# Optimization experiments

Measured on AMD Instinct MI355X. Metric: run time of the kernel, lower is better.

## Reference

```python
import jax, jax.numpy as jnp
import numpy as np

H = 128          # hidden_channels
MID = 64         # middle_channels
NH = 8           # num_heads
HD = H // NH     # head_dim
NS = 20000       # source nodes
NT = 20000       # target nodes
E = 320000       # edges
CUT = 5.0        # cosine cutoff radius
SPHE = 3 * 2 ** 2   # num_radial * num_spherical**2 = 12
TORS = 3 * 2        # num_radial * num_spherical = 6

silu = jax.nn.silu


def setup_inputs() -> dict:
    key = jax.random.key(0)
    ks = jax.random.split(key, 40)
    w = lambda k, shp, s=0.05: (jax.random.normal(k, shp, dtype=jnp.float32) * s)
    inp = {
        "x_s": jax.random.normal(ks[0], (NS, H), dtype=jnp.float32),
        "x_t": jax.random.normal(ks[1], (NT, H), dtype=jnp.float32),
        "edge_index": jnp.stack([
            jax.random.randint(ks[2], (E,), 0, NS),
            jax.random.randint(ks[3], (E,), 0, NT)]).astype(jnp.int32),
        "edge_attr": jax.random.normal(ks[4], (E, H), dtype=jnp.float32),
        "sphe_emb": jax.random.normal(ks[5], (E, SPHE), dtype=jnp.float32),
        "torsion_emb": jax.random.normal(ks[6], (E, TORS), dtype=jnp.float32),
        "dist": jax.random.uniform(ks[7], (E,), dtype=jnp.float32) * 6.0,
        # sphe_proj / torsion_proj (bias-free two-layer MLPs)
        "Ws1": w(ks[8], (SPHE, MID)), "Ws2": w(ks[9], (MID, H)),
        "Wt1": w(ks[10], (TORS, MID)), "Wt2": w(ks[11], (MID, H)),
        # attention projections
        "Wq": w(ks[12], (H, H)), "bq": jnp.zeros((H,), jnp.float32),
        "Wk": w(ks[13], (H, H)), "bk": jnp.zeros((H,), jnp.float32),
        "Wv": w(ks[14], (H, H)), "bv": jnp.zeros((H,), jnp.float32),
        "Wdk": w(ks[15], (H, H)), "bdk": jnp.zeros((H,), jnp.float32),
        "Wdv": w(ks[16], (H, H)), "bdv": jnp.zeros((H,), jnp.float32),
        "Wo_att": w(ks[17], (H, H)), "bo_att": jnp.zeros((H,), jnp.float32),
        # message projections
        "Ws_msg": w(ks[18], (H, 2 * H)), "bs_msg": jnp.zeros((2 * H,), jnp.float32),
        "Wcat_msg": w(ks[19], (2 * H, H)),
        "Wo_msg": w(ks[20], (H, 2 * H)), "bo_msg": jnp.zeros((2 * H,), jnp.float32),
        # final proj (conv_type='inter' -> input is concat([h_t, msg]) of width 2H)
        "Wfinal": w(ks[21], (2 * H, H)), "bfinal": jnp.zeros((H,), jnp.float32),
        # edge update (BaseConv, with_update_edge=True)
        "Wf": w(ks[22], (H, 3 * H)), "bf": jnp.zeros((3 * H,), jnp.float32),
        "Wcat_f": w(ks[23], (2 * H, H)), "bcat_f": jnp.zeros((H,), jnp.float32),
    }
    return inp


def reference(x_s, x_t, edge_index, edge_attr, sphe_emb, torsion_emb, dist,
              Ws1, Ws2, Wt1, Wt2, Wq, bq, Wk, bk, Wv, bv, Wdk, bdk, Wdv, bdv,
              Wo_att, bo_att, Ws_msg, bs_msg, Wcat_msg, Wo_msg, bo_msg,
              Wfinal, bfinal, Wf, bf, Wcat_f, bcat_f):
    src, tgt = edge_index[0], edge_index[1]

    # geometric edge embeddings: [E, H]
    d1 = (sphe_emb @ Ws1) @ Ws2
    d2 = (torsion_emb @ Wt1) @ Wt2

    # multi-head q/k/v
    q = (x_t @ Wq + bq).reshape(-1, NH, HD)
    k = (x_s @ Wk + bk).reshape(-1, NH, HD)
    v = (x_s @ Wv + bv).reshape(-1, NH, HD)
    dk = silu(edge_attr @ Wdk + bdk).reshape(-1, NH, HD)
    dv = silu(edge_attr @ Wdv + bdv).reshape(-1, NH, HD)

    # message: gather per-edge, attention-weighted values
    attn = (q[tgt] * k[src] * dk).sum(-1)                 # [E, NH]
    cut = 0.5 * (jnp.cos(jnp.pi * dist / CUT) + 1.0) * (dist < CUT)
    attn = silu(attn) * cut[:, None]
    v_j = (v[src] * dv * attn[:, :, None]).reshape(-1, H)  # [E, H]
    v_j = silu(v_j @ Wo_att + bo_att)
    s = silu(v_j @ Ws_msg + bs_msg)
    s1, s2 = s[:, :H], s[:, H:]
    d_ji = jnp.concatenate([s1 * d1, s2 * d2], axis=1)      # [E, 2H]

    # scatter-add aggregation to target nodes
    s_msg = jax.ops.segment_sum(v_j, tgt, num_segments=NT)   # [NT, H]
    d_msg = jax.ops.segment_sum(d_ji, tgt, num_segments=NT) @ Wcat_msg  # [NT, H]

    # edge update (BaseConv.edge_update)
    f = silu(edge_attr @ Wf + bf)
    f1, f2, f3 = f[:, :H], f[:, H:2 * H], f[:, 2 * H:]
    f_ji = f1 + silu(jnp.concatenate([f2 * d1, f3 * d2], axis=1) @ Wcat_f + bcat_f)

    # node update (conv_type='inter')
    o = s_msg @ Wo_msg + bo_msg
    s_msg1, s_msg2 = o[:, :H], o[:, H:]
    h_t = silu(jnp.concatenate([x_t, s_msg1 + s_msg2 * d_msg], axis=1) @ Wfinal + bfinal)
    return (h_t, f_ji)
```

## Files before the change

### kernel.cpp

```cpp
#include <hip/hip_runtime.h>
#include <math.h>

static constexpr int H    = 128;
static constexpr int MID  = 64;
static constexpr int NS   = 20000;
static constexpr int NT   = 20000;
static constexpr int EDG  = 320000;
static constexpr int SPH  = 12;
static constexpr int TOR  = 6;
static constexpr int TS   = 132;

typedef unsigned long long u64;
typedef unsigned int u32;
typedef unsigned short ushort_t;

using bf8   = __attribute__((ext_vector_type(8))) short;
using f32x4 = __attribute__((ext_vector_type(4))) float;

__device__ __forceinline__ float sil(float x) {
  return x / (1.0f + __expf(-x));
}

__device__ __forceinline__ ushort_t f2bf(float x) {
  u32 u = __float_as_uint(x);
  u32 r = u + 0x7FFFu + ((u >> 16) & 1u);
  return (ushort_t)(r >> 16);
}
__device__ __forceinline__ float bf2f(ushort_t h) {
  return __uint_as_float(((u32)h) << 16);
}

__device__ __forceinline__ bf8 ld_lds_frag(const char* base, u32 b0, u32 b1) {
  union { u64 u[2]; bf8 v; } X;
  X.u[0] = *(const u64*)(base + b0);
  X.u[1] = *(const u64*)(base + b1);
  return X.v;
}
__device__ __forceinline__ bf8 ld_g_frag(const ushort_t* p) {
  union { u64 u[2]; bf8 v; } X;
  X.u[0] = *(const u64*)(p);
  X.u[1] = *(const u64*)(p + 16);
  return X.v;
}

template<int K>
__device__ __forceinline__ void kloop32(const float* __restrict__ W, int ldw,
                                        const float* xr, float* acc) {
  #pragma unroll 2
  for (int i0 = 0; i0 < K; i0 += 4) {
    float4 a4 = *(const float4*)(xr + i0);
    const float* w = W + i0 * ldw;
    #pragma unroll
    for (int j = 0; j < 32; ++j) acc[j] = fmaf(a4.x, w[j], acc[j]);
    w += ldw;
    #pragma unroll
    for (int j = 0; j < 32; ++j) acc[j] = fmaf(a4.y, w[j], acc[j]);
    w += ldw;
    #pragma unroll
    for (int j = 0; j < 32; ++j) acc[j] = fmaf(a4.z, w[j], acc[j]);
    w += ldw;
    #pragma unroll
    for (int j = 0; j < 32; ++j) acc[j] = fmaf(a4.w, w[j], acc[j]);
  }
}

template<int K>
__device__ __forceinline__ void kloop32x2(const float* __restrict__ Wa,
                                          const float* __restrict__ Wb, int ldw,
                                          const float* xr, float* acca, float* accb) {
  #pragma unroll 2
  for (int i0 = 0; i0 < K; i0 += 4) {
    float4 a4 = *(const float4*)(xr + i0);
    float av[4] = {a4.x, a4.y, a4.z, a4.w};
    #pragma unroll
    for (int u = 0; u < 4; ++u) {
      const float* wa = Wa + (i0 + u) * ldw;
      const float* wb = Wb + (i0 + u) * ldw;
      #pragma unroll
      for (int j = 0; j < 32; ++j) acca[j] = fmaf(av[u], wa[j], acca[j]);
      #pragma unroll
      for (int j = 0; j < 32; ++j) accb[j] = fmaf(av[u], wb[j], accb[j]);
    }
  }
}

__device__ __forceinline__ void flush_seg(const float* __restrict__ X,
                                          const int* __restrict__ Tbuf,
                                          float* __restrict__ out, int ldo, int colbase) {
  int c  = threadIdx.x & 127;
  int r0 = (threadIdx.x >> 7) * 32;
  float acc = X[r0 * TS + c];
  int tcur = Tbuf[r0];
  #pragma unroll 4
  for (int r = r0 + 1; r < r0 + 32; ++r) {
    float v = X[r * TS + c];
    int tn = Tbuf[r];
    if (tn != tcur) {
      atomicAdd(&out[(size_t)tcur * ldo + colbase + c], acc);
      acc = v; tcur = tn;
    } else {
      acc += v;
    }
  }
  atomicAdd(&out[(size_t)tcur * ldo + colbase + c], acc);
}

__global__ void k_hist(const int* __restrict__ ei, int* __restrict__ deg) {
  int e = blockIdx.x * 256 + threadIdx.x;
  if (e < EDG) atomicAdd(&deg[ei[EDG + e]], 1);
}

__global__ void k_scan(const int* __restrict__ deg, int* __restrict__ cursor) {
  __shared__ int part[256];
  int tid = threadIdx.x;
  const int PER = (NT + 255) / 256;
  int base = tid * PER;
  int sum = 0;
  for (int i = 0; i < PER; ++i) {
    int idx = base + i;
    if (idx < NT) sum += deg[idx];
  }
  part[tid] = sum;
  __syncthreads();
  if (tid == 0) {
    int acc = 0;
    for (int i = 0; i < 256; ++i) { int v = part[i]; part[i] = acc; acc += v; }
  }
  __syncthreads();
  int acc = part[tid];
  for (int i = 0; i < PER; ++i) {
    int idx = base + i;
    if (idx < NT) { cursor[idx] = acc; acc += deg[idx]; }
  }
}

__global__ void k_scatter(const int* __restrict__ ei, int* __restrict__ cursor,
                          int* __restrict__ perm) {
  int e = blockIdx.x * 256 + threadIdx.x;
  if (e < EDG) {
    int t = ei[EDG + e];
    int pos = atomicAdd(&cursor[t], 1);
    perm[pos] = e;
  }
}

__global__ void k_smallw(const float* __restrict__ Ws1, const float* __restrict__ Ws2,
                         const float* __restrict__ Wt1, const float* __restrict__ Wt2,
                         float* __restrict__ Wsphe, float* __restrict__ Wtors) {
  int tid = threadIdx.x;
  for (int o = tid; o < SPH * H; o += 256) {
    int i = o >> 7, c = o & 127;
    float acc = 0.f;
    for (int m = 0; m < MID; ++m) acc = fmaf(Ws1[i * MID + m], Ws2[m * H + c], acc);
    Wsphe[o] = acc;
  }
  for (int o = tid; o < TOR * H; o += 256) {
    int i = o >> 7, c = o & 127;
    float acc = 0.f;
    for (int m = 0; m < MID; ++m) acc = fmaf(Wt1[i * MID + m], Wt2[m * H + c], acc);
    Wtors[o] = acc;
  }
}

__global__ void k_prepw(const float* __restrict__ Wf, const float* __restrict__ Wcat_f,
                        const float* __restrict__ Ws1, const float* __restrict__ Ws2,
                        const float* __restrict__ Wt1, const float* __restrict__ Wt2,
                        ushort_t* __restrict__ wfT_hi, ushort_t* __restrict__ wfT_lo,
                        ushort_t* __restrict__ wcatT,
                        ushort_t* __restrict__ wspheT, ushort_t* __restrict__ wtorsT) {
  int idx = blockIdx.x * 256 + threadIdx.x;
  if (idx < 384 * 128) {
    int n = idx >> 7, k = idx & 127;
    float v = Wf[k * 384 + n];
    ushort_t h = f2bf(v);
    wfT_hi[idx] = h;
    wfT_lo[idx] = f2bf(v - bf2f(h));
  }
  if (idx < 128 * 256) {
    int n = idx >> 8, k = idx & 255;
    wcatT[idx] = f2bf(Wcat_f[k * 128 + n]);
  }
  if (idx < 128 * 32) {
    int n = idx >> 5, k = idx & 31;
    float v = 0.f;
    if (k < SPH) {
      for (int m = 0; m < MID; ++m) v = fmaf(Ws1[k * MID + m], Ws2[m * H + n], v);
    }
    wspheT[idx] = f2bf(v);
    float v2 = 0.f;
    if (k < TOR) {
      for (int m = 0; m < MID; ++m) v2 = fmaf(Wt1[k * MID + m], Wt2[m * H + n], v2);
    }
    wtorsT[idx] = f2bf(v2);
  }
}

__global__ __launch_bounds__(256, 4)
void k_gemm128(const float* __restrict__ A, const float* __restrict__ W,
               const float* __restrict__ bias, float* __restrict__ Out, int M) {
  __shared__ float X[64 * TS];
  int tid = threadIdx.x;
  int r0 = blockIdx.x * 64;
  for (int idx = tid; idx < 64 * 32; idx += 256) {
    int r = idx >> 5, seg = idx & 31;
    int row = r0 + r;
    float4 val = make_float4(0.f, 0.f, 0.f, 0.f);
    if (row < M) val = *(const float4*)(A + row * H + seg * 4);
    *(float4*)(X + r * TS + seg * 4) = val;
  }
  __syncthreads();
  int lane = tid & 63, wave = tid >> 6;
  int c0 = __builtin_amdgcn_readfirstlane(wave * 32);
  float acc[32];
  #pragma unroll
  for (int j = 0; j < 32; ++j) acc[j] = bias[c0 + j];
  kloop32<128>(W + c0, H, X + lane * TS, acc);
  int row = r0 + lane;
  if (row < M) {
    #pragma unroll
    for (int j4 = 0; j4 < 8; ++j4) {
      float4 o4 = make_float4(acc[j4*4], acc[j4*4+1], acc[j4*4+2], acc[j4*4+3]);
      *(float4*)(Out + row * H + c0 + j4 * 4) = o4;
    }
  }
}

__global__ __launch_bounds__(256, 4)
void k_edge_attn(const float* __restrict__ edge_attr, const int* __restrict__ ei,
                 const int* __restrict__ perm,
                 const float* __restrict__ sphe, const float* __restrict__ tors,
                 const float* __restrict__ dist,
                 const float* __restrict__ q, const float* __restrict__ kk,
                 const float* __restrict__ vv,
                 const float* __restrict__ Wdk, const float* __restrict__ bdk,
                 const float* __restrict__ Wdv, const float* __restrict__ bdv,
                 const float* __restrict__ Wo_att, const float* __restrict__ bo_att,
                 const float* __restrict__ Ws_msg, const float* __restrict__ bs_msg,
                 const float* __restrict__ Wsphe, const float* __restrict__ Wtors,
                 float* __restrict__ s_msg, float* __restrict__ dsum) {
  __shared__ float X[64 * TS];
  __shared__ int Ebuf[64];
  __shared__ int Tbuf[64];
  int tid = threadIdx.x;
  int b0 = blockIdx.x * 64;
  if (tid < 64) {
    int ee = perm[b0 + tid];
    Ebuf[tid] = ee;
    Tbuf[tid] = ei[EDG + ee];
  }
  __syncthreads();
  for (int idx = tid; idx < 64 * 32; idx += 256) {
    int r = idx >> 5, seg = idx & 31;
    *(float4*)(X + r * TS + seg * 4) =
        *(const float4*)(edge_attr + (size_t)Ebuf[r] * H + seg * 4);
  }
  __syncthreads();
  int lane = tid & 63, wave = tid >> 6;
  int c0 = __builtin_amdgcn_readfirstlane(wave * 32);
  int e = Ebuf[lane];
  int t = Tbuf[lane];
  int s = ei[e];
  const float* xr = X + lane * TS;

  float dk[32], dv[32];
  #pragma unroll
  for (int j = 0; j < 32; ++j) { dk[j] = bdk[c0 + j]; dv[j] = bdv[c0 + j]; }
  kloop32x2<128>(Wdk + c0, Wdv + c0, H, xr, dk, dv);
  #pragma unroll
  for (int j = 0; j < 32; ++j) { dk[j] = sil(dk[j]); dv[j] = sil(dv[j]); }

  float ah0 = 0.f, ah1 = 0.f;
  #pragma unroll
  for (int j8 = 0; j8 < 8; ++j8) {
    float4 q4 = *(const float4*)(q  + (size_t)t * H + c0 + j8 * 4);
    float4 k4 = *(const float4*)(kk + (size_t)s * H + c0 + j8 * 4);
    float p = q4.x * k4.x * dk[j8*4]   + q4.y * k4.y * dk[j8*4+1]
            + q4.z * k4.z * dk[j8*4+2] + q4.w * k4.w * dk[j8*4+3];
    if (j8 < 4) ah0 += p; else ah1 += p;
  }
  float dd = dist[e];
  float cutv = (dd < 5.0f) ? 0.5f * (__cosf(0.6283185307179586f * dd) + 1.0f) : 0.0f;
  float a0 = sil(ah0) * cutv;
  float a1 = sil(ah1) * cutv;

  float vj[32];
  #pragma unroll
  for (int j8 = 0; j8 < 8; ++j8) {
    float4 v4 = *(const float4*)(vv + (size_t)s * H + c0 + j8 * 4);
    float aa = (j8 < 4) ? a0 : a1;
    vj[j8*4]   = v4.x * dv[j8*4]   * aa;
    vj[j8*4+1] = v4.y * dv[j8*4+1] * aa;
    vj[j8*4+2] = v4.z * dv[j8*4+2] * aa;
    vj[j8*4+3] = v4.w * dv[j8*4+3] * aa;
  }
  __syncthreads();
  #pragma unroll
  for (int j4 = 0; j4 < 8; ++j4) {
    float4 o4 = make_float4(vj[j4*4], vj[j4*4+1], vj[j4*4+2], vj[j4*4+3]);
    *(float4*)(X + lane * TS + c0 + j4 * 4) = o4;
  }
  __syncthreads();

  float acc[32];
  #pragma unroll
  for (int j = 0; j < 32; ++j) acc[j] = bo_att[c0 + j];
  kloop32<128>(Wo_att + c0, H, xr, acc);
  #pragma unroll
  for (int j = 0; j < 32; ++j) vj[j] = sil(acc[j]);
  __syncthreads();
  #pragma unroll
  for (int j4 = 0; j4 < 8; ++j4) {
    float4 o4 = make_float4(vj[j4*4], vj[j4*4+1], vj[j4*4+2], vj[j4*4+3]);
    *(float4*)(X + lane * TS + c0 + j4 * 4) = o4;
  }
  __syncthreads();

  flush_seg(X, Tbuf, s_msg, H, 0);

  int c1 = __builtin_amdgcn_readfirstlane(wave * 64);
  float s0[32], s1[32];
  #pragma unroll
  for (int j = 0; j < 32; ++j) { s0[j] = bs_msg[c1 + j]; s1[j] = bs_msg[c1 + 32 + j]; }
  kloop32x2<128>(Ws_msg + c1, Ws_msg + c1 + 32, 2 * H, xr, s0, s1);
  #pragma unroll
  for (int j = 0; j < 32; ++j) { s0[j] = sil(s0[j]); s1[j] = sil(s1[j]); }

  if (wave < 2) {
    const float4* spp = (const float4*)(sphe + (size_t)e * SPH);
    float4 sa = spp[0], sb = spp[1], sc = spp[2];
    float sp[12] = {sa.x, sa.y, sa.z, sa.w, sb.x, sb.y, sb.z, sb.w, sc.x, sc.y, sc.z, sc.w};
    #pragma unroll
    for (int j = 0; j < 32; ++j) {
      float d = 0.f;
      #pragma unroll
      for (int i = 0; i < 12; ++i) d = fmaf(sp[i], Wsphe[i * H + c1 + j], d);
      s0[j] *= d;
    }
    #pragma unroll
    for (int j = 0; j < 32; ++j) {
      float d = 0.f;
      #pragma unroll
      for (int i = 0; i < 12; ++i) d = fmaf(sp[i], Wsphe[i * H + c1 + 32 + j], d);
      s1[j] *= d;
    }
  } else {
    const float* tpp = tors + (size_t)e * TOR;
    float tp[6];
    #pragma unroll
    for (int i = 0; i < 6; ++i) tp[i] = tpp[i];
    int d0 = c1 - 128;
    #pragma unroll
    for (int j = 0; j < 32; ++j) {
      float d = 0.f;
      #pragma unroll
      for (int i = 0; i < 6; ++i) d = fmaf(tp[i], Wtors[i * H + d0 + j], d);
      s0[j] *= d;
    }
    #pragma unroll
    for (int j = 0; j < 32; ++j) {
      float d = 0.f;
      #pragma unroll
      for (int i = 0; i < 6; ++i) d = fmaf(tp[i], Wtors[i * H + d0 + 32 + j], d);
      s1[j] *= d;
    }
  }
  __syncthreads();

  if (wave < 2) {
    #pragma unroll
    for (int j4 = 0; j4 < 8; ++j4) {
      float4 o4 = make_float4(s0[j4*4], s0[j4*4+1], s0[j4*4+2], s0[j4*4+3]);
      *(float4*)(X + lane * TS + c1 + j4 * 4) = o4;
    }
    #pragma unroll
    for (int j4 = 0; j4 < 8; ++j4) {
      float4 o4 = make_float4(s1[j4*4], s1[j4*4+1], s1[j4*4+2], s1[j4*4+3]);
      *(float4*)(X + lane * TS + c1 + 32 + j4 * 4) = o4;
    }
  }
  __syncthreads();
  flush_seg(X, Tbuf, dsum, 2 * H, 0);
  __syncthreads();

  if (wave >= 2) {
    int cb = c1 - 128;
    #pragma unroll
    for (int j4 = 0; j4 < 8; ++j4) {
      float4 o4 = make_float4(s0[j4*4], s0[j4*4+1], s0[j4*4+2], s0[j4*4+3]);
      *(float4*)(X + lane * TS + cb + j4 * 4) = o4;
    }
    #pragma unroll
    for (int j4 = 0; j4 < 8; ++j4) {
      float4 o4 = make_float4(s1[j4*4], s1[j4*4+1], s1[j4*4+2], s1[j4*4+3]);
      *(float4*)(X + lane * TS + cb + 32 + j4 * 4) = o4;
    }
  }
  __syncthreads();
  flush_seg(X, Tbuf, dsum, 2 * H, 128);
}

__global__ __launch_bounds__(256, 1)
void k_edge_f_mfma(const float* __restrict__ edge_attr,
                   const float* __restrict__ sphe, const float* __restrict__ tors,
                   const ushort_t* __restrict__ wfT_hi, const ushort_t* __restrict__ wfT_lo,
                   const ushort_t* __restrict__ wcatT,
                   const ushort_t* __restrict__ wspheT, const ushort_t* __restrict__ wtorsT,
                   const float* __restrict__ bf, const float* __restrict__ bcat_f,
                   float* __restrict__ out_fji) {
  __shared__ __align__(16) ushort_t SH[64 * 256];
  __shared__ __align__(16) ushort_t SpheL[64 * 32];
  __shared__ __align__(16) ushort_t TorsL[64 * 32];
  ushort_t* AhiL = SH;
  ushort_t* AloL = SH + 8192;

  int tid = threadIdx.x;
  int e0  = blockIdx.x * 64;

  {
    int r = tid >> 2, qq = tid & 3;
    const float* src = edge_attr + (size_t)(e0 + r) * H + qq * 32;
    u32 swz = (u32)((r & 7) << 4);
    #pragma unroll
    for (int j = 0; j < 8; ++j) {
      float4 x = *(const float4*)(src + j * 4);
      ushort_t h0 = f2bf(x.x), h1 = f2bf(x.y), h2 = f2bf(x.z), h3 = f2bf(x.w);
      union { ushort_t s[4]; u64 u; } P;
      u32 off = ((u32)(r * 256 + (qq * 32 + j * 4) * 2)) ^ swz;
      P.s[0] = h0; P.s[1] = h1; P.s[2] = h2; P.s[3] = h3;
      *(u64*)((char*)AhiL + off) = P.u;
      P.s[0] = f2bf(x.x - bf2f(h0)); P.s[1] = f2bf(x.y - bf2f(h1));
      P.s[2] = f2bf(x.z - bf2f(h2)); P.s[3] = f2bf(x.w - bf2f(h3));
      *(u64*)((char*)AloL + off) = P.u;
    }
  }
  if (tid < 128) {
    int r = tid & 63;
    bool issp = tid < 64;
    ushort_t vals[32];
    #pragma unroll
    for (int i = 0; i < 32; ++i) vals[i] = 0;
    if (issp) {
      const float* sp = sphe + (size_t)(e0 + r) * SPH;
      #pragma unroll
      for (int i = 0; i < 12; ++i) vals[i] = f2bf(sp[i]);
    } else {
      const float* tp = tors + (size_t)(e0 + r) * TOR;
      #pragma unroll
      for (int i = 0; i < 6; ++i) vals[i] = f2bf(tp[i]);
    }
    ushort_t* dst = issp ? SpheL : TorsL;
    u32 swz = (u32)((r & 7) << 3);
    #pragma unroll
    for (int j = 0; j < 8; ++j) {
      union { ushort_t s[4]; u64 u; } P;
      P.s[0] = vals[j*4]; P.s[1] = vals[j*4+1]; P.s[2] = vals[j*4+2]; P.s[3] = vals[j*4+3];
      u32 off = ((u32)(r * 64 + j * 8)) ^ swz;
      *(u64*)((char*)dst + off) = P.u;
    }
  }
  __syncthreads();

  int lane = tid & 63;
  int w    = tid >> 6;
  int c    = lane & 15;
  int g    = lane >> 4;

  const int ntv[6] = {w, w + 4, 8 + w, 12 + w, 16 + w, 20 + w};

  f32x4 acc[4][6];
  #pragma unroll
  for (int mt = 0; mt < 4; ++mt)
    #pragma unroll
    for (int j = 0; j < 6; ++j) acc[mt][j] = (f32x4){0.f, 0.f, 0.f, 0.f};

  for (int t = 0; t < 4; ++t) {
    bf8 ah[4], al[4];
    #pragma unroll
    for (int mt = 0; mt < 4; ++mt) {
      int row = 16 * mt + c;
      u32 swz = (u32)((row & 7) << 4);
      u32 b0 = ((u32)(row * 256 + t * 64 + g * 8)) ^ swz;
      u32 b1 = ((u32)(row * 256 + t * 64 + 32 + g * 8)) ^ swz;
      ah[mt] = ld_lds_frag((const char*)AhiL, b0, b1);
      al[mt] = ld_lds_frag((const char*)AloL, b0, b1);
    }
    #pragma unroll
    for (int j = 0; j < 6; ++j) {
      int n = 16 * ntv[j] + c;
      bf8 bh = ld_g_frag(wfT_hi + n * 128 + t * 32 + g * 4);
      bf8 bl = ld_g_frag(wfT_lo + n * 128 + t * 32 + g * 4);
      #pragma unroll
      for (int mt = 0; mt < 4; ++mt) {
        acc[mt][j] = __builtin_amdgcn_mfma_f32_16x16x32_bf16(ah[mt], bh, acc[mt][j], 0, 0, 0);
        acc[mt][j] = __builtin_amdgcn_mfma_f32_16x16x32_bf16(al[mt], bh, acc[mt][j], 0, 0, 0);
        acc[mt][j] = __builtin_amdgcn_mfma_f32_16x16x32_bf16(ah[mt], bl, acc[mt][j], 0, 0, 0);
      }
    }
  }
  __syncthreads();

  bf8 spf[4], tof[4];
  #pragma unroll
  for (int mt = 0; mt < 4; ++mt) {
    int row = 16 * mt + c;
    u32 swz = (u32)((row & 7) << 3);
    u32 b0 = ((u32)(row * 64 + g * 8)) ^ swz;
    u32 b1 = ((u32)(row * 64 + 32 + g * 8)) ^ swz;
    spf[mt] = ld_lds_frag((const char*)SpheL, b0, b1);
    tof[mt] = ld_lds_frag((const char*)TorsL, b0, b1);
  }

  float sf1[2][4][4];
  #pragma unroll
  for (int jj = 0; jj < 2; ++jj) {
    float bv = bf[16 * ntv[jj] + c];
    #pragma unroll
    for (int mt = 0; mt < 4; ++mt)
      #pragma unroll
      for (int i = 0; i < 4; ++i)
        sf1[jj][mt][i] = sil(acc[mt][jj][i] + bv);
  }
  #pragma unroll
  for (int jj = 0; jj < 2; ++jj) {
    int j = 2 + jj;
    int nf = ntv[j] - 8;
    float bv = bf[16 * ntv[j] + c];
    bf8 wsf = ld_g_frag(wspheT + (16 * nf + c) * 32 + g * 4);
    #pragma unroll
    for (int mt = 0; mt < 4; ++mt) {
      f32x4 dz = (f32x4){0.f, 0.f, 0.f, 0.f};
      f32x4 d1 = __builtin_amdgcn_mfma_f32_16x16x32_bf16(spf[mt], wsf, dz, 0, 0, 0);
      #pragma unroll
      for (int i = 0; i < 4; ++i) {
        float y = sil(acc[mt][j][i] + bv) * d1[i];
        int row = 16 * mt + 4 * g + i;
        int col = 16 * nf + c;
        u32 off = ((u32)(row * 512 + col * 2)) ^ ((u32)((row & 7) << 4));
        *(ushort_t*)((char*)SH + off) = f2bf(y);
      }
    }
  }
  #pragma unroll
  for (int jj = 0; jj < 2; ++jj) {
    int j = 4 + jj;
    int nf = ntv[j] - 16;
    float bv = bf[16 * ntv[j] + c];
    bf8 wtf = ld_g_frag(wtorsT + (16 * nf + c) * 32 + g * 4);
    #pragma unroll
    for (int mt = 0; mt < 4; ++mt) {
      f32x4 dz = (f32x4){0.f, 0.f, 0.f, 0.f};
      f32x4 d2 = __builtin_amdgcn_mfma_f32_16x16x32_bf16(tof[mt], wtf, dz, 0, 0, 0);
// ... 36 lines not shown
  for (int jj = 0; jj < 2; ++jj) {
    float bc = bcat_f[16 * nt2[jj] + c];
    #pragma unroll
    for (int mt = 0; mt < 4; ++mt) {
      #pragma unroll
      for (int i = 0; i < 4; ++i) {
        int row = 16 * mt + 4 * g + i;
        float v = sf1[jj][mt][i] + sil(acc2[mt][jj][i] + bc);
        out_fji[(size_t)(e0 + row) * H + 16 * nt2[jj] + c] = v;
      }
    }
  }
}

__global__ __launch_bounds__(256, 2)
void k_dmsg(const float* __restrict__ dsum, const float* __restrict__ Wcat_msg,
            float* __restrict__ d_msg) {
  __shared__ float X[64 * 260];
  int tid = threadIdx.x;
  int r0 = blockIdx.x * 64;
  for (int idx = tid; idx < 64 * 64; idx += 256) {
    int r = idx >> 6, seg = idx & 63;
    int row = r0 + r;
    float4 val = make_float4(0.f, 0.f, 0.f, 0.f);
    if (row < NT) val = *(const float4*)(dsum + (size_t)row * 2 * H + seg * 4);
    *(float4*)(X + r * 260 + seg * 4) = val;
  }
  __syncthreads();
  int lane = tid & 63, wave = tid >> 6;
  int c0 = __builtin_amdgcn_readfirstlane(wave * 32);
  float acc[32];
  #pragma unroll
  for (int j = 0; j < 32; ++j) acc[j] = 0.f;
  kloop32<256>(Wcat_msg + c0, H, X + lane * 260, acc);
  int row = r0 + lane;
  if (row < NT) {
    #pragma unroll
    for (int j4 = 0; j4 < 8; ++j4) {
      float4 o4 = make_float4(acc[j4*4], acc[j4*4+1], acc[j4*4+2], acc[j4*4+3]);
      *(float4*)(d_msg + (size_t)row * H + c0 + j4 * 4) = o4;
    }
  }
}

__global__ __launch_bounds__(256, 2)
void k_final(const float* __restrict__ s_msg, const float* __restrict__ x_t,
             const float* __restrict__ d_msg,
             const float* __restrict__ Wo_msg, const float* __restrict__ bo_msg,
             const float* __restrict__ Wfinal, const float* __restrict__ bfinal,
             float* __restrict__ out_ht) {
  __shared__ float SM[64 * TS];
  __shared__ float XT[64 * TS];
  int tid = threadIdx.x;
  int r0 = blockIdx.x * 64;
  for (int idx = tid; idx < 64 * 32; idx += 256) {
    int r = idx >> 5, seg = idx & 31;
    int row = r0 + r;
    float4 v1 = make_float4(0.f, 0.f, 0.f, 0.f), v2 = v1;
    if (row < NT) {
      v1 = *(const float4*)(s_msg + (size_t)row * H + seg * 4);
      v2 = *(const float4*)(x_t   + (size_t)row * H + seg * 4);
    }
    *(float4*)(SM + r * TS + seg * 4) = v1;
    *(float4*)(XT + r * TS + seg * 4) = v2;
  }
  __syncthreads();
  int lane = tid & 63, wave = tid >> 6;
  int c0 = __builtin_amdgcn_readfirstlane(wave * 32);
  int row = r0 + lane;
  float acc1[32], acc2[32];
  #pragma unroll
  for (int j = 0; j < 32; ++j) { acc1[j] = bo_msg[c0 + j]; acc2[j] = bo_msg[H + c0 + j]; }
  kloop32x2<128>(Wo_msg + c0, Wo_msg + H + c0, 2 * H, SM + lane * TS, acc1, acc2);
  float z[32];
  if (row < NT) {
    #pragma unroll
    for (int j4 = 0; j4 < 8; ++j4) {
      float4 dm = *(const float4*)(d_msg + (size_t)row * H + c0 + j4 * 4);
      z[j4*4]   = acc1[j4*4]   + acc2[j4*4]   * dm.x;
      z[j4*4+1] = acc1[j4*4+1] + acc2[j4*4+1] * dm.y;
      z[j4*4+2] = acc1[j4*4+2] + acc2[j4*4+2] * dm.z;
      z[j4*4+3] = acc1[j4*4+3] + acc2[j4*4+3] * dm.w;
    }
  } else {
    #pragma unroll
    for (int j = 0; j < 32; ++j) z[j] = 0.f;
  }
  __syncthreads();
  #pragma unroll
  for (int j4 = 0; j4 < 8; ++j4) {
    float4 o4 = make_float4(z[j4*4], z[j4*4+1], z[j4*4+2], z[j4*4+3]);
    *(float4*)(SM + lane * TS + c0 + j4 * 4) = o4;
  }
  __syncthreads();
  float acc[32];
  #pragma unroll
  for (int j = 0; j < 32; ++j) acc[j] = bfinal[c0 + j];
  kloop32<128>(Wfinal + c0, H, XT + lane * TS, acc);
  kloop32<128>(Wfinal + H * H + c0, H, SM + lane * TS, acc);
  if (row < NT) {
    #pragma unroll
    for (int j4 = 0; j4 < 8; ++j4) {
      float4 o4 = make_float4(sil(acc[j4*4]), sil(acc[j4*4+1]), sil(acc[j4*4+2]), sil(acc[j4*4+3]));
      *(float4*)(out_ht + (size_t)row * H + c0 + j4 * 4) = o4;
    }
  }
}

extern "C" void kernel_launch(void* const* d_in, const int* in_sizes, int n_in,
                              void* d_out, int out_size, void* d_ws, size_t ws_size,
                              hipStream_t stream) {
  const float* x_s       = (const float*)d_in[0];
  const float* x_t       = (const float*)d_in[1];
  const int*   ei        = (const int*)  d_in[2];
  const float* edge_attr = (const float*)d_in[3];
  const float* sphe      = (const float*)d_in[4];
  const float* tors      = (const float*)d_in[5];
  const float* dist      = (const float*)d_in[6];
  const float* Ws1       = (const float*)d_in[7];
  const float* Ws2       = (const float*)d_in[8];
  const float* Wt1       = (const float*)d_in[9];
  const float* Wt2       = (const float*)d_in[10];
  const float* Wq        = (const float*)d_in[11];
  const float* bq        = (const float*)d_in[12];
  const float* Wk        = (const float*)d_in[13];
  const float* bk        = (const float*)d_in[14];
  const float* Wv        = (const float*)d_in[15];
  const float* bv        = (const float*)d_in[16];
  const float* Wdk       = (const float*)d_in[17];
  const float* bdk       = (const float*)d_in[18];
  const float* Wdv       = (const float*)d_in[19];
  const float* bdv       = (const float*)d_in[20];
  const float* Wo_att    = (const float*)d_in[21];
  const float* bo_att    = (const float*)d_in[22];
  const float* Ws_msg    = (const float*)d_in[23];
  const float* bs_msg    = (const float*)d_in[24];
  const float* Wcat_msg  = (const float*)d_in[25];
  const float* Wo_msg    = (const float*)d_in[26];
  const float* bo_msg    = (const float*)d_in[27];
  const float* Wfinal    = (const float*)d_in[28];
  const float* bfinal    = (const float*)d_in[29];
  const float* Wf        = (const float*)d_in[30];
  const float* bf        = (const float*)d_in[31];
  const float* Wcat_f    = (const float*)d_in[32];
  const float* bcat_f    = (const float*)d_in[33];

  float* ws = (float*)d_ws;
  float* qbuf  = ws;
  float* kbuf  = qbuf  + (size_t)NT * H;
  float* vbuf  = kbuf  + (size_t)NS * H;
  float* smsg  = vbuf  + (size_t)NS * H;
  float* dsum  = smsg  + (size_t)NT * H;
  float* dmsg  = dsum  + (size_t)NT * 2 * H;
  float* wsphe = dmsg  + (size_t)NT * H;
  float* wtors = wsphe + SPH * H;
  int*   deg    = (int*)(wtors + TOR * H);
  int*   cursor = deg + NT;
  int*   perm   = cursor + NT;
  ushort_t* wfT_hi = (ushort_t*)(perm + EDG);
  ushort_t* wfT_lo = wfT_hi + 384 * 128;
  ushort_t* wcatT  = wfT_lo + 384 * 128;
  ushort_t* wspheT = wcatT + 128 * 256;
  ushort_t* wtorsT = wspheT + 128 * 32;

  float* out_ht  = (float*)d_out;
  float* out_fji = out_ht + (size_t)NT * H;

  hipMemsetAsync(smsg, 0, (size_t)NT * H * sizeof(float), stream);
  hipMemsetAsync(dsum, 0, (size_t)NT * 2 * H * sizeof(float), stream);
  hipMemsetAsync(deg, 0, (size_t)NT * sizeof(int), stream);

  k_hist<<<(EDG + 255) / 256, 256, 0, stream>>>(ei, deg);
  k_scan<<<1, 256, 0, stream>>>(deg, cursor);
  k_scatter<<<(EDG + 255) / 256, 256, 0, stream>>>(ei, cursor, perm);

  k_smallw<<<1, 256, 0, stream>>>(Ws1, Ws2, Wt1, Wt2, wsphe, wtors);
  k_prepw<<<(384 * 128 + 255) / 256, 256, 0, stream>>>(Wf, Wcat_f, Ws1, Ws2, Wt1, Wt2,
                                                       wfT_hi, wfT_lo, wcatT, wspheT, wtorsT);

  int nblk = (NT + 63) / 64;
  k_gemm128<<<nblk, 256, 0, stream>>>(x_t, Wq, bq, qbuf, NT);
  k_gemm128<<<nblk, 256, 0, stream>>>(x_s, Wk, bk, kbuf, NS);
  k_gemm128<<<nblk, 256, 0, stream>>>(x_s, Wv, bv, vbuf, NS);

  k_edge_attn<<<EDG / 64, 256, 0, stream>>>(edge_attr, ei, perm, sphe, tors, dist,
                                            qbuf, kbuf, vbuf,
                                            Wdk, bdk, Wdv, bdv, Wo_att, bo_att,
                                            Ws_msg, bs_msg, wsphe, wtors,
                                            smsg, dsum);

  k_edge_f_mfma<<<EDG / 64, 256, 0, stream>>>(edge_attr, sphe, tors,
                                              wfT_hi, wfT_lo, wcatT, wspheT, wtorsT,
                                              bf, bcat_f, out_fji);

  k_dmsg<<<nblk, 256, 0, stream>>>(dsum, Wcat_msg, dmsg);

  k_final<<<nblk, 256, 0, stream>>>(smsg, x_t, dmsg, Wo_msg, bo_msg,
                                    Wfinal, bfinal, out_ht);
}
```

Baseline: 2.103 ms.

## Port edge attention kernel GEMMs to bf16 MFMA with hi/lo split precision

Replaces the scalar FP32 register-tiled GEMMs in the edge attention kernel (Wdk, Wdv, Wo_att, Ws_msg, and the sphe/torsion projections) with bf16 MFMA 16x16x32 instructions. Activations and weights are split into bf16 hi/lo pairs and combined with three MFMAs per tile to approximate fp32 accuracy. Weights are pre-transposed and split in the prep kernel, and the separate small-weight kernel is removed. Activations move through swizzled LDS buffers, which raises shared memory use and lowers occupancy (launch bounds drop to 2 blocks per CU).

```diff
diff --git a/kernel.cpp b/kernel.cpp
--- a/kernel.cpp
+++ b/kernel.cpp
@@ -144,30 +144,18 @@
   }
 }
 
-__global__ void k_smallw(const float* __restrict__ Ws1, const float* __restrict__ Ws2,
-                         const float* __restrict__ Wt1, const float* __restrict__ Wt2,
-                         float* __restrict__ Wsphe, float* __restrict__ Wtors) {
-  int tid = threadIdx.x;
-  for (int o = tid; o < SPH * H; o += 256) {
-    int i = o >> 7, c = o & 127;
-    float acc = 0.f;
-    for (int m = 0; m < MID; ++m) acc = fmaf(Ws1[i * MID + m], Ws2[m * H + c], acc);
-    Wsphe[o] = acc;
-  }
-  for (int o = tid; o < TOR * H; o += 256) {
-    int i = o >> 7, c = o & 127;
-    float acc = 0.f;
-    for (int m = 0; m < MID; ++m) acc = fmaf(Wt1[i * MID + m], Wt2[m * H + c], acc);
-    Wtors[o] = acc;
-  }
-}
-
 __global__ void k_prepw(const float* __restrict__ Wf, const float* __restrict__ Wcat_f,
                         const float* __restrict__ Ws1, const float* __restrict__ Ws2,
                         const float* __restrict__ Wt1, const float* __restrict__ Wt2,
+                        const float* __restrict__ Wdk, const float* __restrict__ Wdv,
+                        const float* __restrict__ Wo_att, const float* __restrict__ Ws_msg,
                         ushort_t* __restrict__ wfT_hi, ushort_t* __restrict__ wfT_lo,
                         ushort_t* __restrict__ wcatT,
-                        ushort_t* __restrict__ wspheT, ushort_t* __restrict__ wtorsT) {
+                        ushort_t* __restrict__ wspheT, ushort_t* __restrict__ wtorsT,
+                        ushort_t* __restrict__ wdkT_hi, ushort_t* __restrict__ wdkT_lo,
+                        ushort_t* __restrict__ wdvT_hi, ushort_t* __restrict__ wdvT_lo,
+                        ushort_t* __restrict__ woT_hi, ushort_t* __restrict__ woT_lo,
+                        ushort_t* __restrict__ wsmT_hi, ushort_t* __restrict__ wsmT_lo) {
   int idx = blockIdx.x * 256 + threadIdx.x;
   if (idx < 384 * 128) {
     int n = idx >> 7, k = idx & 127;
@@ -192,6 +180,24 @@
       for (int m = 0; m < MID; ++m) v2 = fmaf(Wt1[k * MID + m], Wt2[m * H + n], v2);
     }
     wtorsT[idx] = f2bf(v2);
+  }
+  if (idx < 128 * 128) {
+    int n = idx >> 7, k = idx & 127;
+    float v = Wdk[k * H + n];
+    ushort_t h = f2bf(v);
+    wdkT_hi[idx] = h; wdkT_lo[idx] = f2bf(v - bf2f(h));
+    v = Wdv[k * H + n];
+    h = f2bf(v);
+    wdvT_hi[idx] = h; wdvT_lo[idx] = f2bf(v - bf2f(h));
+    v = Wo_att[k * H + n];
+    h = f2bf(v);
+    woT_hi[idx] = h; woT_lo[idx] = f2bf(v - bf2f(h));
+  }
+  if (idx < 256 * 128) {
+    int n = idx >> 7, k = idx & 127;
+    float v = Ws_msg[k * 256 + n];
+    ushort_t h = f2bf(v);
+    wsmT_hi[idx] = h; wsmT_lo[idx] = f2bf(v - bf2f(h));
   }
 }
 
@@ -225,178 +231,311 @@
   }
 }
 
-__global__ __launch_bounds__(256, 4)
-void k_edge_attn(const float* __restrict__ edge_attr, const int* __restrict__ ei,
-                 const int* __restrict__ perm,
-                 const float* __restrict__ sphe, const float* __restrict__ tors,
-                 const float* __restrict__ dist,
-                 const float* __restrict__ q, const float* __restrict__ kk,
-                 const float* __restrict__ vv,
-                 const float* __restrict__ Wdk, const float* __restrict__ bdk,
-                 const float* __restrict__ Wdv, const float* __restrict__ bdv,
-                 const float* __restrict__ Wo_att, const float* __restrict__ bo_att,
-                 const float* __restrict__ Ws_msg, const float* __restrict__ bs_msg,
-                 const float* __restrict__ Wsphe, const float* __restrict__ Wtors,
-                 float* __restrict__ s_msg, float* __restrict__ dsum) {
-  __shared__ float X[64 * TS];
-  __shared__ int Ebuf[64];
-  __shared__ int Tbuf[64];
+__global__ __launch_bounds__(256, 2)
+void k_edge_attn_mfma(const float* __restrict__ edge_attr, const int* __restrict__ ei,
+                      const int* __restrict__ perm,
+                      const float* __restrict__ sphe, const float* __restrict__ tors,
+                      const float* __restrict__ dist,
+                      const float* __restrict__ q, const float* __restrict__ kk,
+                      const float* __restrict__ vv,
+                      const ushort_t* __restrict__ wdkT_hi, const ushort_t* __restrict__ wdkT_lo,
+                      const ushort_t* __restrict__ wdvT_hi, const ushort_t* __restrict__ wdvT_lo,
+                      const ushort_t* __restrict__ woT_hi, const ushort_t* __restrict__ woT_lo,
+                      const ushort_t* __restrict__ wsmT_hi, const ushort_t* __restrict__ wsmT_lo,
+                      const ushort_t* __restrict__ wspheT, const ushort_t* __restrict__ wtorsT,
+                      const float* __restrict__ bdk, const float* __restrict__ bdv,
+                      const float* __restrict__ bo_att, const float* __restrict__ bs_msg,
+                      float* __restrict__ s_msg, float* __restrict__ dsum) {
+  __shared__ __align__(16) ushort_t AHs[8192];
+  __shared__ __align__(16) ushort_t ALs[8192];
+  __shared__ __align__(16) float Bb[64 * TS];
+  __shared__ float ATT[64 * 8];
+  __shared__ __align__(16) ushort_t SpheL[2048];
+  __shared__ __align__(16) ushort_t TorsL[2048];
+  __shared__ int Ebuf[64], Tbuf[64], Sbuf[64];
+
   int tid = threadIdx.x;
-  int b0 = blockIdx.x * 64;
+  int b0i = blockIdx.x * 64;
   if (tid < 64) {
-    int ee = perm[b0 + tid];
+    int ee = perm[b0i + tid];
     Ebuf[tid] = ee;
     Tbuf[tid] = ei[EDG + ee];
-  }
-  __syncthreads();
-  for (int idx = tid; idx < 64 * 32; idx += 256) {
-    int r = idx >> 5, seg = idx & 31;
-    *(float4*)(X + r * TS + seg * 4) =
-        *(const float4*)(edge_attr + (size_t)Ebuf[r] * H + seg * 4);
-  }
-  __syncthreads();
-  int lane = tid & 63, wave = tid >> 6;
-  int c0 = __builtin_amdgcn_readfirstlane(wave * 32);
-  int e = Ebuf[lane];
-  int t = Tbuf[lane];
-  int s = ei[e];
-  const float* xr = X + lane * TS;
-
-  float dk[32], dv[32];
-  #pragma unroll
-  for (int j = 0; j < 32; ++j) { dk[j] = bdk[c0 + j]; dv[j] = bdv[c0 + j]; }
-  kloop32x2<128>(Wdk + c0, Wdv + c0, H, xr, dk, dv);
-  #pragma unroll
-  for (int j = 0; j < 32; ++j) { dk[j] = sil(dk[j]); dv[j] = sil(dv[j]); }
-
-  float ah0 = 0.f, ah1 = 0.f;
-  #pragma unroll
-  for (int j8 = 0; j8 < 8; ++j8) {
-    float4 q4 = *(const float4*)(q  + (size_t)t * H + c0 + j8 * 4);
-    float4 k4 = *(const float4*)(kk + (size_t)s * H + c0 + j8 * 4);
-    float p = q4.x * k4.x * dk[j8*4]   + q4.y * k4.y * dk[j8*4+1]
-            + q4.z * k4.z * dk[j8*4+2] + q4.w * k4.w * dk[j8*4+3];
-    if (j8 < 4) ah0 += p; else ah1 += p;
-  }
-  float dd = dist[e];
-  float cutv = (dd < 5.0f) ? 0.5f * (__cosf(0.6283185307179586f * dd) + 1.0f) : 0.0f;
-  float a0 = sil(ah0) * cutv;
-  float a1 = sil(ah1) * cutv;
-
-  float vj[32];
-  #pragma unroll
-  for (int j8 = 0; j8 < 8; ++j8) {
-    float4 v4 = *(const float4*)(vv + (size_t)s * H + c0 + j8 * 4);
-    float aa = (j8 < 4) ? a0 : a1;
-    vj[j8*4]   = v4.x * dv[j8*4]   * aa;
-    vj[j8*4+1] = v4.y * dv[j8*4+1] * aa;
-    vj[j8*4+2] = v4.z * dv[j8*4+2] * aa;
-    vj[j8*4+3] = v4.w * dv[j8*4+3] * aa;
-  }
-  __syncthreads();
-  #pragma unroll
-  for (int j4 = 0; j4 < 8; ++j4) {
-    float4 o4 = make_float4(vj[j4*4], vj[j4*4+1], vj[j4*4+2], vj[j4*4+3]);
-    *(float4*)(X + lane * TS + c0 + j4 * 4) = o4;
-  }
-  __syncthreads();
-
-  float acc[32];
-  #pragma unroll
-  for (int j = 0; j < 32; ++j) acc[j] = bo_att[c0 + j];
-  kloop32<128>(Wo_att + c0, H, xr, acc);
-  #pragma unroll
-  for (int j = 0; j < 32; ++j) vj[j] = sil(acc[j]);
-  __syncthreads();
-  #pragma unroll
-  for (int j4 = 0; j4 < 8; ++j4) {
-    float4 o4 = make_float4(vj[j4*4], vj[j4*4+1], vj[j4*4+2], vj[j4*4+3]);
-    *(float4*)(X + lane * TS + c0 + j4 * 4) = o4;
-  }
-  __syncthreads();
-
-  flush_seg(X, Tbuf, s_msg, H, 0);
-
-  int c1 = __builtin_amdgcn_readfirstlane(wave * 64);
-  float s0[32], s1[32];
-  #pragma unroll
-  for (int j = 0; j < 32; ++j) { s0[j] = bs_msg[c1 + j]; s1[j] = bs_msg[c1 + 32 + j]; }
-  kloop32x2<128>(Ws_msg + c1, Ws_msg + c1 + 32, 2 * H, xr, s0, s1);
-  #pragma unroll
-  for (int j = 0; j < 32; ++j) { s0[j] = sil(s0[j]); s1[j] = sil(s1[j]); }
-
-  if (wave < 2) {
-    const float4* spp = (const float4*)(sphe + (size_t)e * SPH);
-    float4 sa = spp[0], sb = spp[1], sc = spp[2];
-    float sp[12] = {sa.x, sa.y, sa.z, sa.w, sb.x, sb.y, sb.z, sb.w, sc.x, sc.y, sc.z, sc.w};
-    #pragma unroll
-    for (int j = 0; j < 32; ++j) {
-      float d = 0.f;
-      #pragma unroll
-      for (int i = 0; i < 12; ++i) d = fmaf(sp[i], Wsphe[i * H + c1 + j], d);
-      s0[j] *= d;
-    }
-    #pragma unroll
-    for (int j = 0; j < 32; ++j) {
-      float d = 0.f;
-      #pragma unroll
-      for (int i = 0; i < 12; ++i) d = fmaf(sp[i], Wsphe[i * H + c1 + 32 + j], d);
-      s1[j] *= d;
-    }
-  } else {
-    const float* tpp = tors + (size_t)e * TOR;
-    float tp[6];
-    #pragma unroll
-    for (int i = 0; i < 6; ++i) tp[i] = tpp[i];
-    int d0 = c1 - 128;
-    #pragma unroll
-    for (int j = 0; j < 32; ++j) {
-      float d = 0.f;
-      #pragma unroll
-      for (int i = 0; i < 6; ++i) d = fmaf(tp[i], Wtors[i * H + d0 + j], d);
-      s0[j] *= d;
-    }
-    #pragma unroll
-    for (int j = 0; j < 32; ++j) {
-      float d = 0.f;
-      #pragma unroll
-      for (int i = 0; i < 6; ++i) d = fmaf(tp[i], Wtors[i * H + d0 + 32 + j], d);
-      s1[j] *= d;
-    }
-  }
-  __syncthreads();
-
-  if (wave < 2) {
-    #pragma unroll
-    for (int j4 = 0; j4 < 8; ++j4) {
-      float4 o4 = make_float4(s0[j4*4], s0[j4*4+1], s0[j4*4+2], s0[j4*4+3]);
-      *(float4*)(X + lane * TS + c1 + j4 * 4) = o4;
-    }
-    #pragma unroll
-    for (int j4 = 0; j4 < 8; ++j4) {
-      float4 o4 = make_float4(s1[j4*4], s1[j4*4+1], s1[j4*4+2], s1[j4*4+3]);
-      *(float4*)(X + lane * TS + c1 + 32 + j4 * 4) = o4;
-    }
-  }
-  __syncthreads();
-  flush_seg(X, Tbuf, dsum, 2 * H, 0);
-  __syncthreads();
-
-  if (wave >= 2) {
-    int cb = c1 - 128;
-    #pragma unroll
-    for (int j4 = 0; j4 < 8; ++j4) {
-      float4 o4 = make_float4(s0[j4*4], s0[j4*4+1], s0[j4*4+2], s0[j4*4+3]);
-      *(float4*)(X + lane * TS + cb + j4 * 4) = o4;
-    }
-    #pragma unroll
-    for (int j4 = 0; j4 < 8; ++j4) {
-      float4 o4 = make_float4(s1[j4*4], s1[j4*4+1], s1[j4*4+2], s1[j4*4+3]);
-      *(float4*)(X + lane * TS + cb + 32 + j4 * 4) = o4;
-    }
-  }
-  __syncthreads();
-  flush_seg(X, Tbuf, dsum, 2 * H, 128);
+    Sbuf[tid] = ei[ee];
+  }
+  __syncthreads();
+
+  {
+    int r = tid >> 2, qq = tid & 3;
+    const float* src = edge_attr + (size_t)Ebuf[r] * H + qq * 32;
+    u32 swz = (u32)((r & 7) << 4);
+    #pragma unroll
+    for (int j = 0; j < 8; ++j) {
+      float4 x = *(const float4*)(src + j * 4);
+      ushort_t h0 = f2bf(x.x), h1 = f2bf(x.y), h2 = f2bf(x.z), h3 = f2bf(x.w);
+      union { ushort_t s[4]; u64 u; } P;
+      u32 off = ((u32)(r * 256 + (qq * 32 + j * 4) * 2)) ^ swz;
+      P.s[0] = h0; P.s[1] = h1; P.s[2] = h2; P.s[3] = h3;
+      *(u64*)((char*)AHs + off) = P.u;
+      P.s[0] = f2bf(x.x - bf2f(h0)); P.s[1] = f2bf(x.y - bf2f(h1));
+      P.s[2] = f2bf(x.z - bf2f(h2)); P.s[3] = f2bf(x.w - bf2f(h3));
+      *(u64*)((char*)ALs + off) = P.u;
+    }
+  }
+  if (tid < 128) {
+    int r = tid & 63;
+    bool issp = tid < 64;
+    ushort_t vals[32];
+    #pragma unroll
+    for (int i = 0; i < 32; ++i) vals[i] = 0;
+    if (issp) {
+      const float* sp = sphe + (size_t)Ebuf[r] * SPH;
+      #pragma unroll
+      for (int i = 0; i < 12; ++i) vals[i] = f2bf(sp[i]);
+    } else {
+      const float* tp = tors + (size_t)Ebuf[r] * TOR;
+      #pragma unroll
+      for (int i = 0; i < 6; ++i) vals[i] = f2bf(tp[i]);
+    }
+    ushort_t* dst = issp ? SpheL : TorsL;
+    u32 swz = (u32)((r & 7) << 3);
+    #pragma unroll
+    for (int j = 0; j < 8; ++j) {
+      union { ushort_t s[4]; u64 u; } P;
+      P.s[0] = vals[j*4]; P.s[1] = vals[j*4+1]; P.s[2] = vals[j*4+2]; P.s[3] = vals[j*4+3];
+      u32 off = ((u32)(r * 64 + j * 8)) ^ swz;
+      *(u64*)((char*)dst + off) = P.u;
+    }
+  }
+  __syncthreads();
+
+  int lane = tid & 63, w = tid >> 6;
+  int c = lane & 15, g = lane >> 4;
+
+  f32x4 ak[4][2], av[4][2];
+  #pragma unroll
+  for (int mt = 0; mt < 4; ++mt)
+    #pragma unroll
+    for (int jj = 0; jj < 2; ++jj) {
+      ak[mt][jj] = (f32x4){0.f,0.f,0.f,0.f};
+      av[mt][jj] = (f32x4){0.f,0.f,0.f,0.f};
+    }
+  for (int t = 0; t < 4; ++t) {
+    bf8 ah[4], al[4];
+    #pragma unroll
+    for (int mt = 0; mt < 4; ++mt) {
+      int row = 16 * mt + c;
+      u32 swz = (u32)((row & 7) << 4);
+      u32 o0 = ((u32)(row * 256 + t * 64 + g * 8)) ^ swz;
+      u32 o1 = ((u32)(row * 256 + t * 64 + 32 + g * 8)) ^ swz;
+      ah[mt] = ld_lds_frag((const char*)AHs, o0, o1);
+      al[mt] = ld_lds_frag((const char*)ALs, o0, o1);
+    }
+    #pragma unroll
+    for (int jj = 0; jj < 2; ++jj) {
+      int n = 16 * (2 * w + jj) + c;
+      const ushort_t* pk = wdkT_hi + n * 128 + t * 32 + g * 4;
+      const ushort_t* pkl = wdkT_lo + n * 128 + t * 32 + g * 4;
+      const ushort_t* pv = wdvT_hi + n * 128 + t * 32 + g * 4;
+      const ushort_t* pvl = wdvT_lo + n * 128 + t * 32 + g * 4;
+      bf8 bhk = ld_g_frag(pk), blk = ld_g_frag(pkl);
+      bf8 bhv = ld_g_frag(pv), blv = ld_g_frag(pvl);
+      #pragma unroll
+      for (int mt = 0; mt < 4; ++mt) {
+        ak[mt][jj] = __builtin_amdgcn_mfma_f32_16x16x32_bf16(ah[mt], bhk, ak[mt][jj], 0, 0, 0);
+        ak[mt][jj] = __builtin_amdgcn_mfma_f32_16x16x32_bf16(al[mt], bhk, ak[mt][jj], 0, 0, 0);
+        ak[mt][jj] = __builtin_amdgcn_mfma_f32_16x16x32_bf16(ah[mt], blk, ak[mt][jj], 0, 0, 0);
+        av[mt][jj] = __builtin_amdgcn_mfma_f32_16x16x32_bf16(ah[mt], bhv, av[mt][jj], 0, 0, 0);
+        av[mt][jj] = __builtin_amdgcn_mfma_f32_16x16x32_bf16(al[mt], bhv, av[mt][jj], 0, 0, 0);
+        av[mt][jj] = __builtin_amdgcn_mfma_f32_16x16x32_bf16(ah[mt], blv, av[mt][jj], 0, 0, 0);
+      }
+    }
+  }
+  #pragma unroll
+  for (int jj = 0; jj < 2; ++jj) {
+    int col = 32 * w + 16 * jj + c;
+    float bv = bdk[col];
+    #pragma unroll
+    for (int mt = 0; mt < 4; ++mt)
+      #pragma unroll
+      for (int i = 0; i < 4; ++i)
+        Bb[(16 * mt + 4 * g + i) * TS + col] = sil(ak[mt][jj][i] + bv);
+  }
+
+  {
+    int e = Ebuf[lane], tt = Tbuf[lane], ss = Sbuf[lane];
+    int c0 = w * 32;
+    float ah0 = 0.f, ah1 = 0.f;
+    #pragma unroll
+    for (int j8 = 0; j8 < 8; ++j8) {
+      float4 q4 = *(const float4*)(q  + (size_t)tt * H + c0 + j8 * 4);
+      float4 k4 = *(const float4*)(kk + (size_t)ss * H + c0 + j8 * 4);
+      float4 d4 = *(const float4*)(Bb + lane * TS + c0 + j8 * 4);
+      float p = q4.x * k4.x * d4.x + q4.y * k4.y * d4.y
+              + q4.z * k4.z * d4.z + q4.w * k4.w * d4.w;
+      if (j8 < 4) ah0 += p; else ah1 += p;
+    }
+    float dd = dist[e];
+    float cutv = (dd < 5.0f) ? 0.5f * (__cosf(0.6283185307179586f * dd) + 1.0f) : 0.0f;
+    ATT[lane * 8 + 2 * w]     = sil(ah0) * cutv;
+    ATT[lane * 8 + 2 * w + 1] = sil(ah1) * cutv;
+  }
+  __syncthreads();
+
+  #pragma unroll
+  for (int jj = 0; jj < 2; ++jj) {
+    int col = 32 * w + 16 * jj + c;
+    float bv = bdv[col];
+    #pragma unroll
+    for (int mt = 0; mt < 4; ++mt) {
+      #pragma unroll
+      for (int i = 0; i < 4; ++i) {
+        int row = 16 * mt + 4 * g + i;
+        float att = ATT[row * 8 + 2 * w + jj];
+        float vval = vv[(size_t)Sbuf[row] * H + col];
+        float y = sil(av[mt][jj][i] + bv) * att * vval;
+        ushort_t h = f2bf(y);
+        u32 off = ((u32)(row * 256 + col * 2)) ^ ((u32)((row & 7) << 4));
+        *(ushort_t*)((char*)AHs + off) = h;
+        *(ushort_t*)((char*)ALs + off) = f2bf(y - bf2f(h));
+      }
+    }
+  }
+  __syncthreads();
+
+  f32x4 a2[4][2];
+  #pragma unroll
+  for (int mt = 0; mt < 4; ++mt) { a2[mt][0] = (f32x4){0.f,0.f,0.f,0.f}; a2[mt][1] = (f32x4){0.f,0.f,0.f,0.f}; }
+  for (int t = 0; t < 4; ++t) {
+    bf8 ah[4], al[4];
+    #pragma unroll
+    for (int mt = 0; mt < 4; ++mt) {
+      int row = 16 * mt + c;
+      u32 swz = (u32)((row & 7) << 4);
+      u32 o0 = ((u32)(row * 256 + t * 64 + g * 8)) ^ swz;
+      u32 o1 = ((u32)(row * 256 + t * 64 + 32 + g * 8)) ^ swz;
+      ah[mt] = ld_lds_frag((const char*)AHs, o0, o1);
+      al[mt] = ld_lds_frag((const char*)ALs, o0, o1);
+    }
+    #pragma unroll
+    for (int jj = 0; jj < 2; ++jj) {
+      int n = 16 * (2 * w + jj) + c;
+      bf8 bh = ld_g_frag(woT_hi + n * 128 + t * 32 + g * 4);
+      bf8 bl = ld_g_frag(woT_lo + n * 128 + t * 32 + g * 4);
+      #pragma unroll
+      for (int mt = 0; mt < 4; ++mt) {
+        a2[mt][jj] = __builtin_amdgcn_mfma_f32_16x16x32_bf16(ah[mt], bh, a2[mt][jj], 0, 0, 0);
+        a2[mt][jj] = __builtin_amdgcn_mfma_f32_16x16x32_bf16(al[mt], bh, a2[mt][jj], 0, 0, 0);
+        a2[mt][jj] = __builtin_amdgcn_mfma_f32_16x16x32_bf16(ah[mt], bl, a2[mt][jj], 0, 0, 0);
+      }
+    }
+  }
+  __syncthreads();
+
+  #pragma unroll
+  for (int jj = 0; jj < 2; ++jj) {
+    int col = 32 * w + 16 * jj + c;
+    float bv = bo_att[col];
+    #pragma unroll
+    for (int mt = 0; mt < 4; ++mt) {
+      #pragma unroll
+      for (int i = 0; i < 4; ++i) {
+        int row = 16 * mt + 4 * g + i;
+        float y = sil(a2[mt][jj][i] + bv);
+        Bb[row * TS + col] = y;
+        ushort_t h = f2bf(y);
+        u32 off = ((u32)(row * 256 + col * 2)) ^ ((u32)((row & 7) << 4));
+        *(ushort_t*)((char*)AHs + off) = h;
+        *(ushort_t*)((char*)ALs + off) = f2bf(y - bf2f(h));
+      }
+    }
+  }
+  __syncthreads();
+
+  flush_seg(Bb, Tbuf, s_msg, H, 0);
+
+  const int nt3[4] = {w, 4 + w, 8 + w, 12 + w};
+  f32x4 a3[4][4];
+  #pragma unroll
+  for (int mt = 0; mt < 4; ++mt)
+    #pragma unroll
+    for (int jj = 0; jj < 4; ++jj) a3[mt][jj] = (f32x4){0.f,0.f,0.f,0.f};
+  for (int t = 0; t < 4; ++t) {
+    bf8 ah[4], al[4];
+    #pragma unroll
+    for (int mt = 0; mt < 4; ++mt) {
+      int row = 16 * mt + c;
+      u32 swz = (u32)((row & 7) << 4);
+      u32 o0 = ((u32)(row * 256 + t * 64 + g * 8)) ^ swz;
+      u32 o1 = ((u32)(row * 256 + t * 64 + 32 + g * 8)) ^ swz;
+      ah[mt] = ld_lds_frag((const char*)AHs, o0, o1);
+      al[mt] = ld_lds_frag((const char*)ALs, o0, o1);
+    }
+    #pragma unroll
+    for (int jj = 0; jj < 4; ++jj) {
+      int n = 16 * nt3[jj] + c;
+      bf8 bh = ld_g_frag(wsmT_hi + n * 128 + t * 32 + g * 4);
+      bf8 bl = ld_g_frag(wsmT_lo + n * 128 + t * 32 + g * 4);
+      #pragma unroll
+      for (int mt = 0; mt < 4; ++mt) {
+        a3[mt][jj] = __builtin_amdgcn_mfma_f32_16x16x32_bf16(ah[mt], bh, a3[mt][jj], 0, 0, 0);
+        a3[mt][jj] = __builtin_amdgcn_mfma_f32_16x16x32_bf16(al[mt], bh, a3[mt][jj], 0, 0, 0);
+        a3[mt][jj] = __builtin_amdgcn_mfma_f32_16x16x32_bf16(ah[mt], bl, a3[mt][jj], 0, 0, 0);
+      }
+    }
+  }
+
+  bf8 spf[4], tof[4];
+  #pragma unroll
+  for (int mt = 0; mt < 4; ++mt) {
+    int row = 16 * mt + c;
+    u32 swz = (u32)((row & 7) << 3);
+    u32 o0 = ((u32)(row * 64 + g * 8)) ^ swz;
+    u32 o1 = ((u32)(row * 64 + 32 + g * 8)) ^ swz;
+    spf[mt] = ld_lds_frag((const char*)SpheL, o0, o1);
+    tof[mt] = ld_lds_frag((const char*)TorsL, o0, o1);
+  }
+
+  __syncthreads();
+  #pragma unroll
+  for (int jj = 0; jj < 2; ++jj) {
+    int tj = nt3[jj];
+    int col = 16 * tj + c;
+    float bv = bs_msg[col];
+    bf8 wsf = ld_g_frag(wspheT + col * 32 + g * 4);
+    #pragma unroll
+    for (int mt = 0; mt < 4; ++mt) {
+      f32x4 dz = (f32x4){0.f,0.f,0.f,0.f};
+      f32x4 d1 = __builtin_amdgcn_mfma_f32_16x16x32_bf16(spf[mt], wsf, dz, 0, 0, 0);
+      #pragma unroll
+      for (int i = 0; i < 4; ++i) {
+        int row = 16 * mt + 4 * g + i;
+        Bb[row * TS + col] = sil(a3[mt][jj][i] + bv) * d1[i];
+      }
+    }
+  }
+  __syncthreads();
+  flush_seg(Bb, Tbuf, dsum, 2 * H, 0);
+  __syncthreads();
+
+  #pragma unroll
+  for (int jj = 2; jj < 4; ++jj) {
+    int tj = nt3[jj];
+    int gcol = 16 * tj + c;
+    float bv = bs_msg[gcol];
+    bf8 wtf = ld_g_frag(wtorsT + (gcol - 128) * 32 + g * 4);
+    #pragma unroll
+    for (int mt = 0; mt < 4; ++mt) {
+      f32x4 dz = (f32x4){0.f,0.f,0.f,0.f};
+      f32x4 d2 = __builtin_amdgcn_mfma_f32_16x16x32_bf16(tof[mt], wtf, dz, 0, 0, 0);
+      #pragma unroll
+      for (int i = 0; i < 4; ++i) {
+        int row = 16 * mt + 4 * g + i;
+        Bb[row * TS + (gcol - 128)] = sil(a3[mt][jj][i] + bv) * d2[i];
+      }
+    }
+  }
+  __syncthreads();
+  flush_seg(Bb, Tbuf, dsum, 2 * H, 128);
 }
 
 __global__ __launch_bounds__(256, 1)
@@ -739,16 +878,22 @@
   float* smsg  = vbuf  + (size_t)NS * H;
   float* dsum  = smsg  + (size_t)NT * H;
   float* dmsg  = dsum  + (size_t)NT * 2 * H;
-  float* wsphe = dmsg  + (size_t)NT * H;
-  float* wtors = wsphe + SPH * H;
-  int*   deg    = (int*)(wtors + TOR * H);
+  int*   deg    = (int*)(dmsg + (size_t)NT * H);
   int*   cursor = deg + NT;
   int*   perm   = cursor + NT;
-  ushort_t* wfT_hi = (ushort_t*)(perm + EDG);
-  ushort_t* wfT_lo = wfT_hi + 384 * 128;
-  ushort_t* wcatT  = wfT_lo + 384 * 128;
-  ushort_t* wspheT = wcatT + 128 * 256;
-  ushort_t* wtorsT = wspheT + 128 * 32;
+  ushort_t* wfT_hi  = (ushort_t*)(perm + EDG);
+  ushort_t* wfT_lo  = wfT_hi + 384 * 128;
+  ushort_t* wcatT   = wfT_lo + 384 * 128;
+  ushort_t* wspheT  = wcatT + 128 * 256;
+  ushort_t* wtorsT  = wspheT + 128 * 32;
+  ushort_t* wdkT_hi = wtorsT + 128 * 32;
+  ushort_t* wdkT_lo = wdkT_hi + 128 * 128;
+  ushort_t* wdvT_hi = wdkT_lo + 128 * 128;
+  ushort_t* wdvT_lo = wdvT_hi + 128 * 128;
+  ushort_t* woT_hi  = wdvT_lo + 128 * 128;
+  ushort_t* woT_lo  = woT_hi + 128 * 128;
+  ushort_t* wsmT_hi = woT_lo + 128 * 128;
+  ushort_t* wsmT_lo = wsmT_hi + 256 * 128;
 
   float* out_ht  = (float*)d_out;
   float* out_fji = out_ht + (size_t)NT * H;
@@ -761,20 +906,20 @@
   k_scan<<<1, 256, 0, stream>>>(deg, cursor);
   k_scatter<<<(EDG + 255) / 256, 256, 0, stream>>>(ei, cursor, perm);
 
-  k_smallw<<<1, 256, 0, stream>>>(Ws1, Ws2, Wt1, Wt2, wsphe, wtors);
-  k_prepw<<<(384 * 128 + 255) / 256, 256, 0, stream>>>(Wf, Wcat_f, Ws1, Ws2, Wt1, Wt2,
-                                                       wfT_hi, wfT_lo, wcatT, wspheT, wtorsT);
+  k_prepw<<<(384 * 128 + 255) / 256, 256, 0, stream>>>(
+      Wf, Wcat_f, Ws1, Ws2, Wt1, Wt2, Wdk, Wdv, Wo_att, Ws_msg,
+      wfT_hi, wfT_lo, wcatT, wspheT, wtorsT,
+      wdkT_hi, wdkT_lo, wdvT_hi, wdvT_lo, woT_hi, woT_lo, wsmT_hi, wsmT_lo);
 
   int nblk = (NT + 63) / 64;
   k_gemm128<<<nblk, 256, 0, stream>>>(x_t, Wq, bq, qbuf, NT);
   k_gemm128<<<nblk, 256, 0, stream>>>(x_s, Wk, bk, kbuf, NS);
   k_gemm128<<<nblk, 256, 0, stream>>>(x_s, Wv, bv, vbuf, NS);
 
-  k_edge_attn<<<EDG / 64, 256, 0, stream>>>(edge_attr, ei, perm, sphe, tors, dist,
-                                            qbuf, kbuf, vbuf,
-                                            Wdk, bdk, Wdv, bdv, Wo_att, bo_att,
-                                            Ws_msg, bs_msg, wsphe, wtors,
-                                            smsg, dsum);
+  k_edge_attn_mfma<<<EDG / 64, 256, 0, stream>>>(
+      edge_attr, ei, perm, sphe, tors, dist, qbuf, kbuf, vbuf,
+      wdkT_hi, wdkT_lo, wdvT_hi, wdvT_lo, woT_hi, woT_lo, wsmT_hi, wsmT_lo,
+      wspheT, wtorsT, bdk, bdv, bo_att, bs_msg, smsg, dsum);
 
   k_edge_f_mfma<<<EDG / 64, 256, 0, stream>>>(edge_attr, sphe, tors,
                                               wfT_hi, wfT_lo, wcatT, wspheT, wtorsT,
```

After: 1.720 ms. 18.2% less time.
